# Performance work log

Hardware: AMD Instinct MI355X
Metric: run time of the kernel (lower is better)

Reference implementation:

```python
import jax, jax.numpy as jnp
import numpy as np

TEMPERATURE = 1.0
STRIDE = 1
PADDING = 2
RF = 5  # receptive_field_size
TREE_DEPTH = 3

# Each of the 16 binary difflogic ops op_g(a,b) is multilinear:
# op_g = c0 + c1*a + c2*b + c3*a*b. Rows ordered per the standard difflogic table:
# 0:0, 1:a&b, 2:a&~b, 3:a, 4:~a&b, 5:b, 6:xor, 7:or, 8:nor, 9:xnor,
# 10:~b, 11:a|~b, 12:~a, 13:~a|b, 14:nand, 15:1
_C = jnp.asarray(np.array([
    [0, 0, 0, 0],
    [0, 0, 0, 1],
    [0, 1, 0, -1],
    [0, 1, 0, 0],
    [0, 0, 1, -1],
    [0, 0, 1, 0],
    [0, 1, 1, -2],
    [0, 1, 1, -1],
    [1, -1, -1, 1],
    [1, -1, -1, 2],
    [1, 0, -1, 0],
    [1, 0, -1, 1],
    [1, -1, 0, 0],
    [1, -1, 0, 1],
    [1, 0, 0, -1],
    [1, 0, 0, 0]], dtype=np.float32))


def _gate(a, b, logits):
    """Soft LUT gate. a,b: (B,K,N,P); logits: (N,K,16) -> (B,K,N,P)."""
    w = jax.nn.softmax(logits / TEMPERATURE, axis=-1)          # (N,K,16)
    coef = jnp.einsum('nkg,gc->knc', w, _C)                    # (K,N,4)
    c = coef[None, :, :, None, :]                              # (1,K,N,1,4)
    return c[..., 0] + c[..., 1] * a + c[..., 2] * b + c[..., 3] * (a * b)


def setup_inputs() -> dict:
    key = jax.random.key(0)
    ks = jax.random.split(key, 8)
    B, Cin, H, W = 16, 32, 64, 64
    K, N = 64, 2 ** TREE_DEPTH  # num_kernels, leaf gates per tree
    x = jax.random.uniform(ks[0], (B, Cin, H, W), dtype=jnp.float32)
    idx_h = jax.random.randint(ks[1], (2, K, N), 0, RF, dtype=jnp.int32)
    idx_w = jax.random.randint(ks[2], (2, K, N), 0, RF, dtype=jnp.int32)
    idx_c = jax.random.randint(ks[3], (2, K, N), 0, Cin, dtype=jnp.int32)
    w0 = jax.random.normal(ks[4], (8, K, 16), dtype=jnp.float32)
    w1 = jax.random.normal(ks[5], (4, K, 16), dtype=jnp.float32)
    w2 = jax.random.normal(ks[6], (2, K, 16), dtype=jnp.float32)
    w3 = jax.random.normal(ks[7], (1, K, 16), dtype=jnp.float32)
    return {"x": x, "idx_h": idx_h, "idx_w": idx_w, "idx_c": idx_c,
            "w0": w0, "w1": w1, "w2": w2, "w3": w3}


def reference(x, idx_h, idx_w, idx_c, w0, w1, w2, w3):
    B, Cin, H, W = x.shape
    xp = jnp.pad(x, ((0, 0), (0, 0), (PADDING, PADDING), (PADDING, PADDING)))
    out_h = (H + 2 * PADDING - RF) // STRIDE + 1
    out_w = (W + 2 * PADDING - RF) // STRIDE + 1
    # Absolute gather coords per (rank-slot, kernel, leaf-gate, out_y, out_x)
    abs_h = idx_h[..., None, None] + (jnp.arange(out_h) * STRIDE)[:, None]   # (2,K,N,oh,1)
    abs_w = idx_w[..., None, None] + (jnp.arange(out_w) * STRIDE)[None, :]   # (2,K,N,1,ow)
    cc = idx_c[..., None, None]                                              # (2,K,N,1,1)
    g = xp[:, cc, abs_h, abs_w]                                # (B,2,K,N,oh,ow)
    K, N = g.shape[2], g.shape[3]
    g = g.reshape(B, 2, K, N, out_h * out_w)                   # (B,2,K,N,P)
    cur = _gate(g[:, 0], g[:, 1], w0)                          # (B,K,8,P) leaf level
    for wl in (w1, w2, w3):                                    # reduce tree: 8->4->2->1
        cur = _gate(cur[:, :, 0::2, :], cur[:, :, 1::2, :], wl)
    return cur.reshape(B, K, out_h, out_w)
```

## Files before the change

### kernel.cpp

```cpp
#include <hip/hip_runtime.h>
#include <hip/hip_bf16.h>

#define CIN 32
#define HW 64
#define KK 64
#define NLEAF 8
#define PADDING 2
#define TH 4
#define TCW 16
#define WR 8
#define WC 20
#define WPOS (CIN * WR * WC)

typedef float f32x2 __attribute__((ext_vector_type(2)));
typedef float f32x4 __attribute__((ext_vector_type(4)));

__device__ __constant__ float d_C[16][4] = {
    {0, 0, 0, 0},  {0, 0, 0, 1},  {0, 1, 0, -1}, {0, 1, 0, 0},
    {0, 0, 1, -1}, {0, 0, 1, 0},  {0, 1, 1, -2}, {0, 1, 1, -1},
    {1, -1, -1, 1},{1, -1, -1, 2},{1, 0, -1, 0}, {1, 0, -1, 1},
    {1, -1, 0, 0}, {1, -1, 0, 1}, {1, 0, 0, -1}, {1, 0, 0, 0}
};

__global__ __launch_bounds__(256) void prep_kernel(
    const int* __restrict__ idx_h, const int* __restrict__ idx_w, const int* __restrict__ idx_c,
    const float* __restrict__ w0, const float* __restrict__ w1,
    const float* __restrict__ w2, const float* __restrict__ w3,
    float* __restrict__ coefA, int* __restrict__ loffA)
{
    int tid = blockIdx.x * 256 + threadIdx.x;

    {
        int k = tid >> 4, n = tid & 15;
        int s = n >> 3, leaf = n & 7;
        int o = s * (KK * NLEAF) + k * NLEAF + leaf;
        loffA[tid] = (idx_c[o] * (WR * WC) + idx_h[o] * WC + idx_w[o]) * 16;
    }

    if (tid < KK * 15) {
        int k = tid / 15, node = tid % 15;
        const float* wp; int n;
        if (node < 8)       { wp = w0; n = node; }
        else if (node < 12) { wp = w1; n = node - 8; }
        else if (node < 14) { wp = w2; n = node - 12; }
        else                { wp = w3; n = 0; }
        const float4* lp = (const float4*)(wp + (size_t)(n * KK + k) * 16);
        float4 L0 = lp[0], L1 = lp[1], L2 = lp[2], L3 = lp[3];
        float l[16] = {L0.x, L0.y, L0.z, L0.w, L1.x, L1.y, L1.z, L1.w,
                       L2.x, L2.y, L2.z, L2.w, L3.x, L3.y, L3.z, L3.w};
        float m = l[0];
        #pragma unroll
        for (int g = 1; g < 16; ++g) m = fmaxf(m, l[g]);
        float p[16], s = 0.f;
        #pragma unroll
        for (int g = 0; g < 16; ++g) { p[g] = __expf(l[g] - m); s += p[g]; }
        float inv = 1.f / s;
        float c0 = 0, c1 = 0, c2 = 0, c3 = 0;
        #pragma unroll
        for (int g = 0; g < 16; ++g) {
            float w = p[g] * inv;
            c0 = fmaf(w, d_C[g][0], c0);
            c1 = fmaf(w, d_C[g][1], c1);
            c2 = fmaf(w, d_C[g][2], c2);
            c3 = fmaf(w, d_C[g][3], c3);
        }
        float* o = coefA + (k * 60 + node * 4);
        o[0] = c0; o[1] = c1; o[2] = c2; o[3] = c3;
    }
}

__device__ __forceinline__ f32x2 bc(float s) { return (f32x2){s, s}; }
__device__ __forceinline__ f32x2 gate2(const float* c, f32x2 a, f32x2 b) {
    return __builtin_elementwise_fma(b,
               __builtin_elementwise_fma(a, bc(c[3]), bc(c[2])),
               __builtin_elementwise_fma(a, bc(c[1]), bc(c[0])));
}

__global__ __launch_bounds__(512, 4) void logic_conv_kernel(
    const float* __restrict__ x, const int* __restrict__ loffA,
    const float* __restrict__ coefA, float* __restrict__ out)
{
    extern __shared__ f32x4 xt[];

    int tid  = threadIdx.x;
    int grp  = blockIdx.x & 7;
    int quad = grp & 3;
    int kh   = grp >> 2;
    int t    = blockIdx.x >> 3;
    int r0   = (t >> 2) * TH;
    int c0   = (t & 3) * TCW;

    int lane = tid & 63, wave = tid >> 6;
    int kbase = __builtin_amdgcn_readfirstlane(kh * 32 + wave * 4);
    int tr = lane >> 4, tc = lane & 15;
    int pxb = (tr * WC + tc) * 16;

    int ga[4][16];
    #pragma unroll
    for (int j = 0; j < 4; ++j) {
        const int* L = loffA + ((kbase + j) << 4);
        #pragma unroll
        for (int n = 0; n < 16; ++n)
            ga[j][n] = L[n] + pxb;
    }

    const float* xb0 = x + (size_t)(4 * quad) * (CIN * HW * HW);
    const float* xb1 = xb0 + (CIN * HW * HW);
    const float* xb2 = xb1 + (CIN * HW * HW);
    const float* xb3 = xb2 + (CIN * HW * HW);

    #pragma unroll
    for (int i = 0; i < 10; ++i) {
        int e  = tid + i * 512;
        int c  = e / (WR * WC);
        int r  = e - c * (WR * WC);
        int rr = r / WC;
        int cc = r - rr * WC;
        int ih = r0 + rr - PADDING, iw = c0 + cc - PADDING;
        f32x4 v = {0.f, 0.f, 0.f, 0.f};
        if ((unsigned)ih < HW && (unsigned)iw < HW) {
            int go = (c * HW + ih) * HW + iw;
            v.x = xb0[go];
            v.y = xb1[go];
            v.z = xb2[go];
            v.w = xb3[go];
        }
        xt[e] = v;
    }
    __syncthreads();

    int pxout = (r0 + tr) * HW + (c0 + tc);
    float* outB0 = out + ((size_t)(4 * quad) << 18);
    float* outB1 = outB0 + (1 << 18);
    float* outB2 = outB1 + (1 << 18);
    float* outB3 = outB2 + (1 << 18);
    const char* xtb = (const char*)xt;

    #pragma unroll
    for (int j = 0; j < 4; ++j) {
        const float* C = coefA + (kbase + j) * 60;

        f32x2 gA[16], gB[16];
        #pragma unroll
        for (int n = 0; n < 16; ++n) {
            f32x4 gv = *(const f32x4*)(xtb + ga[j][n]);
            gA[n] = (f32x2){gv.x, gv.y};
            gB[n] = (f32x2){gv.z, gv.w};
        }

        f32x2 vA[8], vB[8];
        #pragma unroll
        for (int n = 0; n < 8; ++n) {
            vA[n] = gate2(C + 4 * n, gA[n], gA[8 + n]);
            vB[n] = gate2(C + 4 * n, gB[n], gB[8 + n]);
        }
        f32x2 uA[4], uB[4];
        #pragma unroll
        for (int n = 0; n < 4; ++n) {
            uA[n] = gate2(C + 32 + 4 * n, vA[2 * n], vA[2 * n + 1]);
            uB[n] = gate2(C + 32 + 4 * n, vB[2 * n], vB[2 * n + 1]);
        }
        f32x2 sA0 = gate2(C + 48, uA[0], uA[1]);
        f32x2 sA1 = gate2(C + 52, uA[2], uA[3]);
        f32x2 sB0 = gate2(C + 48, uB[0], uB[1]);
        f32x2 sB1 = gate2(C + 52, uB[2], uB[3]);
        f32x2 qA  = gate2(C + 56, sA0, sA1);
        f32x2 qB  = gate2(C + 56, sB0, sB1);

        int ko = ((kbase + j) << 12) + pxout;
        __builtin_nontemporal_store(qA.x, &outB0[ko]);
        __builtin_nontemporal_store(qA.y, &outB1[ko]);
        __builtin_nontemporal_store(qB.x, &outB2[ko]);
        __builtin_nontemporal_store(qB.y, &outB3[ko]);
    }
}

extern "C" void kernel_launch(void* const* d_in, const int* in_sizes, int n_in,
                              void* d_out, int out_size, void* d_ws, size_t ws_size,
                              hipStream_t stream) {
    const float* x     = (const float*)d_in[0];
    const int*   idx_h = (const int*)d_in[1];
    const int*   idx_w = (const int*)d_in[2];
    const int*   idx_c = (const int*)d_in[3];
    const float* w0    = (const float*)d_in[4];
    const float* w1    = (const float*)d_in[5];
    const float* w2    = (const float*)d_in[6];
    const float* w3    = (const float*)d_in[7];
    float* out   = (float*)d_out;

    float* coefA = (float*)d_ws;
    int*   loffA = (int*)((char*)d_ws + 16384);

    hipLaunchKernelGGL(prep_kernel, dim3(4), dim3(256), 0, stream,
                       idx_h, idx_w, idx_c, w0, w1, w2, w3, coefA, loffA);
    hipLaunchKernelGGL(logic_conv_kernel, dim3(512), dim3(512),
                       WPOS * sizeof(f32x4), stream,
                       x, loffA, coefA, out);
}
```

Before: 21.27 us.

## Pre-pad and interleave input in prep kernel, stage tiles via global_load_lds

The prep kernel now writes a zero-padded copy of x into workspace, with four batch images interleaved as float4 per pixel. The main kernel then fills its shared-memory tile with direct global-to-LDS loads (global_load_lds, 16 bytes) instead of bounds-checked scalar loads and register round trips. This removes the padding branches and per-thread staging work in the conv kernel. In exchange it adds a full extra write and read of the padded input (about 9.5 MB) in a much larger prep launch.

Measured after the change: 23.15 us. +8.8%, slower.

```diff
diff --git a/kernel.cpp b/kernel.cpp
--- a/kernel.cpp
+++ b/kernel.cpp
@@ -11,6 +11,10 @@
 #define WR 8
 #define WC 20
 #define WPOS (CIN * WR * WC)
+#define PW 68
+#define PIMG (PW * PW)
+#define NP4 (4 * CIN * PIMG)
+#define NPADBLK 578
 
 typedef float f32x2 __attribute__((ext_vector_type(2)));
 typedef float f32x4 __attribute__((ext_vector_type(4)));
@@ -23,22 +27,50 @@
 };
 
 __global__ __launch_bounds__(256) void prep_kernel(
+    const float* __restrict__ x,
     const int* __restrict__ idx_h, const int* __restrict__ idx_w, const int* __restrict__ idx_c,
     const float* __restrict__ w0, const float* __restrict__ w1,
     const float* __restrict__ w2, const float* __restrict__ w3,
-    float* __restrict__ coefA, int* __restrict__ loffA)
+    float* __restrict__ coefA, int* __restrict__ loffA, f32x4* __restrict__ xpad4)
 {
-    int tid = blockIdx.x * 256 + threadIdx.x;
+    int blk = blockIdx.x;
+    if (blk < NPADBLK) {
+        int t = blk * 256 + threadIdx.x;
+        #pragma unroll
+        for (int it = 0; it < 4; ++it) {
+            int e = t + it * (NPADBLK * 256);
+            if (e < NP4) {
+                int qc = e / PIMG;
+                int r  = e - qc * PIMG;
+                int q  = qc >> 5, c = qc & 31;
+                int ph = r / PW;
+                int pw = r - ph * PW;
+                int ih = ph - PADDING, iw = pw - PADDING;
+                f32x4 v = {0.f, 0.f, 0.f, 0.f};
+                if ((unsigned)ih < HW && (unsigned)iw < HW) {
+                    const float* xb = x + ((size_t)(4 * q) * CIN + c) * (HW * HW)
+                                    + ih * HW + iw;
+                    v.x = xb[0];
+                    v.y = xb[CIN * HW * HW];
+                    v.z = xb[2 * CIN * HW * HW];
+                    v.w = xb[3 * CIN * HW * HW];
+                }
+                xpad4[e] = v;
+            }
+        }
+        return;
+    }
+    int t = (blk - NPADBLK) * 256 + threadIdx.x;
 
     {
-        int k = tid >> 4, n = tid & 15;
+        int k = t >> 4, n = t & 15;
         int s = n >> 3, leaf = n & 7;
         int o = s * (KK * NLEAF) + k * NLEAF + leaf;
-        loffA[tid] = (idx_c[o] * (WR * WC) + idx_h[o] * WC + idx_w[o]) * 16;
-    }
-
-    if (tid < KK * 15) {
-        int k = tid / 15, node = tid % 15;
+        loffA[t] = (idx_c[o] * (WR * WC) + idx_h[o] * WC + idx_w[o]) * 16;
+    }
+
+    if (t < KK * 15) {
+        int k = t / 15, node = t % 15;
         const float* wp; int n;
         if (node < 8)       { wp = w0; n = node; }
         else if (node < 12) { wp = w1; n = node - 8; }
@@ -77,7 +109,7 @@
 }
 
 __global__ __launch_bounds__(512, 4) void logic_conv_kernel(
-    const float* __restrict__ x, const int* __restrict__ loffA,
+    const f32x4* __restrict__ xpad4, const int* __restrict__ loffA,
     const float* __restrict__ coefA, float* __restrict__ out)
 {
     extern __shared__ f32x4 xt[];
@@ -92,9 +124,26 @@
 
     int lane = tid & 63, wave = tid >> 6;
     int kbase = __builtin_amdgcn_readfirstlane(kh * 32 + wave * 4);
+
+    const f32x4* xq = xpad4 + (size_t)quad * (CIN * PIMG);
+
+    #pragma unroll
+    for (int i = 0; i < 10; ++i) {
+        int e  = wave * 640 + i * 64 + lane;
+        int c  = e / (WR * WC);
+        int r  = e - c * (WR * WC);
+        int rr = r / WC;
+        int cc = r - rr * WC;
+        const f32x4* gsrc = xq + (c * PIMG + (r0 + rr) * PW + (c0 + cc));
+        f32x4* ldst = xt + (wave * 640 + i * 64);
+        __builtin_amdgcn_global_load_lds(
+            (const __attribute__((address_space(1))) void*)gsrc,
+            (__attribute__((address_space(3))) void*)ldst,
+            16, 0, 0);
+    }
+
     int tr = lane >> 4, tc = lane & 15;
     int pxb = (tr * WC + tc) * 16;
-
     int ga[4][16];
     #pragma unroll
     for (int j = 0; j < 4; ++j) {
@@ -104,29 +153,6 @@
             ga[j][n] = L[n] + pxb;
     }
 
-    const float* xb0 = x + (size_t)(4 * quad) * (CIN * HW * HW);
-    const float* xb1 = xb0 + (CIN * HW * HW);
-    const float* xb2 = xb1 + (CIN * HW * HW);
-    const float* xb3 = xb2 + (CIN * HW * HW);
-
-    #pragma unroll
-    for (int i = 0; i < 10; ++i) {
-        int e  = tid + i * 512;
-        int c  = e / (WR * WC);
-        int r  = e - c * (WR * WC);
-        int rr = r / WC;
-        int cc = r - rr * WC;
-        int ih = r0 + rr - PADDING, iw = c0 + cc - PADDING;
-        f32x4 v = {0.f, 0.f, 0.f, 0.f};
-        if ((unsigned)ih < HW && (unsigned)iw < HW) {
-            int go = (c * HW + ih) * HW + iw;
-            v.x = xb0[go];
-            v.y = xb1[go];
-            v.z = xb2[go];
-            v.w = xb3[go];
-        }
-        xt[e] = v;
-    }
     __syncthreads();
 
     int pxout = (r0 + tr) * HW + (c0 + tc);
@@ -186,14 +212,16 @@
     const float* w1    = (const float*)d_in[5];
     const float* w2    = (const float*)d_in[6];
     const float* w3    = (const float*)d_in[7];
-    float* out   = (float*)d_out;
+    float* out = (float*)d_out;
 
     float* coefA = (float*)d_ws;
     int*   loffA = (int*)((char*)d_ws + 16384);
-
-    hipLaunchKernelGGL(prep_kernel, dim3(4), dim3(256), 0, stream,
-                       idx_h, idx_w, idx_c, w0, w1, w2, w3, coefA, loffA);
+    f32x4* xpad4 = (f32x4*)((char*)d_ws + 32768);
+
+    hipLaunchKernelGGL(prep_kernel, dim3(NPADBLK + 4), dim3(256), 0, stream,
+                       x, idx_h, idx_w, idx_c, w0, w1, w2, w3,
+                       coefA, loffA, xpad4);
     hipLaunchKernelGGL(logic_conv_kernel, dim3(512), dim3(512),
                        WPOS * sizeof(f32x4), stream,
-                       x, loffA, coefA, out);
-}
+                       xpad4, loffA, coefA, out);
+}
```
